# Kernel tuning notes

Hardware: AMD Instinct MI355X
Metric: run time of the kernel (lower is better)

The kernel has to match this reference:

```python
import jax, jax.numpy as jnp
import numpy as np

NUM_HEADS = 16
EPS = 1e-6
ROPE_BASE = 10000.0

def _thw(N, TT):
    table = {2640: (3, 22, 40), 1530: (3, 17, 30), 6120: (3, 34, 60), 660: (3, 11, 20)}
    return table.get(N - TT, (3, 23, 40))

def _positions(t, h, w):
    tt, hh, ww = np.meshgrid(np.arange(t), np.arange(h), np.arange(w), indexing='ij')
    return jnp.asarray(np.stack([tt, hh, ww], -1).reshape(-1, 3), jnp.float32)  # (THW, 3)

def _rope1d(x, pos):
    # x: (B,H,T,d) one axis-chunk, pos: (T,) positions for that axis
    d = x.shape[-1]
    inv_freq = 1.0 / (ROPE_BASE ** (jnp.arange(0, d, 2, dtype=jnp.float32) / d))
    ang = pos[:, None] * inv_freq                     # (T, d/2)
    cos = jnp.concatenate([jnp.cos(ang)] * 2, -1)     # (T, d)
    sin = jnp.concatenate([jnp.sin(ang)] * 2, -1)
    x1, x2 = x[..., : d // 2], x[..., d // 2:]
    return x * cos + jnp.concatenate([-x2, x1], -1) * sin

def _rope3d(x, pos, TT):
    # first TT tokens (text) pass through; video tokens get per-axis rotation
    pre, vid = x[:, :, :TT], x[:, :, TT:]
    chunks = jnp.split(vid, 3, axis=-1)               # t/h/w axis chunks
    rot = [_rope1d(c, pos[:, i]) for i, c in enumerate(chunks)]
    return jnp.concatenate([pre, jnp.concatenate(rot, -1)], axis=2)

def _rms(x, w):
    return x * jax.lax.rsqrt(jnp.mean(x * x, -1, keepdims=True) + EPS) * w

def setup_inputs() -> dict:
    key = jax.random.key(0)
    ks = jax.random.split(key, 12)
    B, N, C = 1, 2866, 1536
    Dh = C // NUM_HEADS
    s = 0.02
    return {
        'x': jax.random.normal(ks[0], (B, N, C), jnp.float32),
        'Wq': jax.random.normal(ks[1], (C, C), jnp.float32) * s,
        'bq': jnp.zeros((C,), jnp.float32),
        'Wk': jax.random.normal(ks[2], (C, C), jnp.float32) * s,
        'bk': jnp.zeros((C,), jnp.float32),
        'Wv': jax.random.normal(ks[3], (C, C), jnp.float32) * s,
        'bv': jnp.zeros((C,), jnp.float32),
        'qn_w': jnp.ones((Dh,), jnp.float32),
        'kn_w': jnp.ones((Dh,), jnp.float32),
        'Wp': jax.random.normal(ks[4], (C, C), jnp.float32) * s,
        'bp': jnp.zeros((C,), jnp.float32),
        'TT': 226,
    }

def reference(x, Wq, bq, Wk, bk, Wv, bv, qn_w, kn_w, Wp, bp, TT):
    B, N, C = x.shape
    H = NUM_HEADS
    Dh = C // H
    def proj(W, b):
        return (x @ W.T + b).reshape(B, N, H, Dh).transpose(0, 2, 1, 3)  # (B,H,N,Dh)
    q, k, v = proj(Wq, bq), proj(Wk, bk), proj(Wv, bv)
    q, k = _rms(q, qn_w), _rms(k, kn_w)
    t, h, w = _thw(N, TT)
    pos = _positions(t, h, w)
    q = _rope3d(q, pos, TT)
    k = _rope3d(k, pos, TT)
    scale = Dh ** -0.5
    attn = jax.nn.softmax(jnp.einsum('bhqd,bhkd->bhqk', q, k) * scale, axis=-1)
    o = jnp.einsum('bhqk,bhkd->bhqd', attn, v)
    o = o.transpose(0, 2, 1, 3).reshape(B, N, C)
    return o @ Wp.T + bp
```

## Files before the change

### kernel.cpp

```cpp
#include <hip/hip_runtime.h>
#include <hip/hip_bf16.h>
#include <math.h>

#define C_DIM 1536
#define H_NUM 16
#define DH    96

typedef __attribute__((ext_vector_type(4))) float  f32x4;
typedef __attribute__((ext_vector_type(8))) short  bf16x8;

__device__ __forceinline__ unsigned short f2bf_rne(float f) {
    unsigned u = __float_as_uint(f);
    unsigned r = (u + 0x7FFFu + ((u >> 16) & 1u)) >> 16;
    return (unsigned short)r;
}
__device__ __forceinline__ float bf2f(unsigned short h) {
    return __uint_as_float(((unsigned)h) << 16);
}

__device__ __forceinline__ void glds16(const void* g, void* l) {
    __builtin_amdgcn_global_load_lds(
        (const __attribute__((address_space(1))) unsigned int*)g,
        (__attribute__((address_space(3))) unsigned int*)l, 16, 0, 0);
}

__global__ __launch_bounds__(256)
void cvt_split(const float* __restrict__ in, unsigned short* __restrict__ hi,
               unsigned short* __restrict__ lo, int n4)
{
    const int i = blockIdx.x * 256 + threadIdx.x;
    if (i >= n4) return;
    float4 v = *(const float4*)&in[4 * i];
    unsigned short h[4], l[4];
    float vv[4] = {v.x, v.y, v.z, v.w};
    #pragma unroll
    for (int j = 0; j < 4; ++j) {
        h[j] = f2bf_rne(vv[j]);
        l[j] = f2bf_rne(vv[j] - bf2f(h[j]));
    }
    *(ushort4*)&hi[4 * i] = *(ushort4*)h;
    *(ushort4*)&lo[4 * i] = *(ushort4*)l;
}

struct CvtArgs {
    const float* src[4];
    unsigned short* hi[4];
    unsigned short* lo[4];
};
__global__ __launch_bounds__(256)
void cvt_split4(CvtArgs a, int n4)
{
    const int i = blockIdx.x * 256 + threadIdx.x;
    if (i >= n4) return;
    const int w = blockIdx.y;
    float4 v = *(const float4*)&a.src[w][4 * i];
    unsigned short h[4], l[4];
    float vv[4] = {v.x, v.y, v.z, v.w};
    #pragma unroll
    for (int j = 0; j < 4; ++j) {
        h[j] = f2bf_rne(vv[j]);
        l[j] = f2bf_rne(vv[j] - bf2f(h[j]));
    }
    *(ushort4*)&a.hi[w][4 * i] = *(ushort4*)h;
    *(ushort4*)&a.lo[w][4 * i] = *(ushort4*)l;
}

__global__ __launch_bounds__(256)
void gemm_mfma(const unsigned short* __restrict__ Ahi,
               const unsigned short* __restrict__ Alo,
               const unsigned short* W0h, const unsigned short* W0l,
               const float* b0, float* Y0,
               const unsigned short* W1h, const unsigned short* W1l,
               const float* b1, float* Y1,
               const unsigned short* W2h, const unsigned short* W2l,
               const float* b2, float* Y2,
               int M)
{
    __shared__ __align__(16) unsigned short lds[2 * 4 * 4096];

    const unsigned short* Wh;
    const unsigned short* Wl;
    const float* bias;
    float* Y;
    if (blockIdx.z == 0)      { Wh = W0h; Wl = W0l; bias = b0; Y = Y0; }
    else if (blockIdx.z == 1) { Wh = W1h; Wl = W1l; bias = b1; Y = Y1; }
    else                      { Wh = W2h; Wl = W2l; bias = b2; Y = Y2; }

    const int t   = threadIdx.x;
    const int m0  = blockIdx.x * 128;
    const int n0  = blockIdx.y * 128;
    const int w   = t >> 6;
    const int l   = t & 63;

    const unsigned short* src =
        (w == 0) ? Ahi : (w == 1) ? Alo : (w == 2) ? Wh : Wl;
    const int rbase = (w < 2) ? m0 : n0;
    const int rmax  = (w < 2) ? (M - 1) : 0x3FFFFFFF;
    const int srow  = l >> 2;
    const int scol  = l & 3;
    const int ssw   = (srow >> 1) & 3;
    int goff[8];
    #pragma unroll
    for (int i = 0; i < 8; ++i) {
        int gr = rbase + 16 * i + srow;
        gr = gr < rmax ? gr : rmax;
        goff[i] = gr * C_DIM + 8 * (scol ^ ssw);
    }

    const int lane = t & 63;
    const int wv   = t >> 6;
    const int wm   = wv & 1, wn = wv >> 1;
    const int lrow = lane & 15;
    const int quad = lane >> 4;
    const int pc   = quad ^ ((lrow >> 1) & 3);
    int aoff[4], boff[4];
    #pragma unroll
    for (int i = 0; i < 4; ++i) {
        aoff[i] = (64 * wm + 16 * i + lrow) * 32 + 8 * pc;
        boff[i] = (64 * wn + 16 * i + lrow) * 32 + 8 * pc;
    }

    f32x4 acc[4][4];
    #pragma unroll
    for (int i = 0; i < 4; ++i)
        #pragma unroll
        for (int j = 0; j < 4; ++j) acc[i][j] = (f32x4)0.f;

    #pragma unroll
    for (int i = 0; i < 8; ++i)
        glds16(src + goff[i], (char*)&lds[w * 4096] + i * 1024);

    const int NT = C_DIM / 32;
    for (int kt = 0; kt < NT; ++kt) {
        const int cb = kt & 1;
        const unsigned short* sA = lds + cb * 16384;

        asm volatile("s_waitcnt vmcnt(0)" ::: "memory");
        __builtin_amdgcn_s_barrier();
        __builtin_amdgcn_sched_barrier(0);

        bf16x8 ah[2], al[2], bh[4], bl[4];

        if (kt + 1 < NT) {
            char* dN = (char*)&lds[(cb ^ 1) * 16384 + w * 4096];
            const int k0n = (kt + 1) * 32;
            #pragma unroll
            for (int i = 0; i < 8; ++i)
                glds16(src + goff[i] + k0n, dN + i * 1024);
        }
        #pragma unroll
        for (int j = 0; j < 4; ++j) {
            bh[j] = *(const bf16x8*)&sA[8192 + boff[j]];
            bl[j] = *(const bf16x8*)&sA[12288 + boff[j]];
        }
        #pragma unroll
        for (int i = 0; i < 2; ++i) {
            ah[i] = *(const bf16x8*)&sA[aoff[i]];
            al[i] = *(const bf16x8*)&sA[4096 + aoff[i]];
        }
        __builtin_amdgcn_s_barrier();
        asm volatile("s_waitcnt lgkmcnt(0)" ::: "memory");
        __builtin_amdgcn_sched_barrier(0);
        __builtin_amdgcn_s_setprio(1);
        #pragma unroll
        for (int i = 0; i < 2; ++i)
            #pragma unroll
            for (int j = 0; j < 4; ++j) {
                acc[i][j] = __builtin_amdgcn_mfma_f32_16x16x32_bf16(ah[i], bh[j], acc[i][j], 0, 0, 0);
                acc[i][j] = __builtin_amdgcn_mfma_f32_16x16x32_bf16(al[i], bh[j], acc[i][j], 0, 0, 0);
                acc[i][j] = __builtin_amdgcn_mfma_f32_16x16x32_bf16(ah[i], bl[j], acc[i][j], 0, 0, 0);
            }
        __builtin_amdgcn_s_setprio(0);
        __builtin_amdgcn_s_barrier();
        __builtin_amdgcn_sched_barrier(0);

        #pragma unroll
        for (int i = 0; i < 2; ++i) {
            ah[i] = *(const bf16x8*)&sA[aoff[2 + i]];
            al[i] = *(const bf16x8*)&sA[4096 + aoff[2 + i]];
        }
        __builtin_amdgcn_s_barrier();
        asm volatile("s_waitcnt lgkmcnt(0)" ::: "memory");
        __builtin_amdgcn_sched_barrier(0);
        __builtin_amdgcn_s_setprio(1);
        #pragma unroll
        for (int i = 0; i < 2; ++i)
            #pragma unroll
            for (int j = 0; j < 4; ++j) {
                acc[2 + i][j] = __builtin_amdgcn_mfma_f32_16x16x32_bf16(ah[i], bh[j], acc[2 + i][j], 0, 0, 0);
                acc[2 + i][j] = __builtin_amdgcn_mfma_f32_16x16x32_bf16(al[i], bh[j], acc[2 + i][j], 0, 0, 0);
                acc[2 + i][j] = __builtin_amdgcn_mfma_f32_16x16x32_bf16(ah[i], bl[j], acc[2 + i][j], 0, 0, 0);
            }
        __builtin_amdgcn_s_setprio(0);
    }

    float bv[4];
    #pragma unroll
    for (int j = 0; j < 4; ++j) bv[j] = bias[n0 + 64 * wn + 16 * j + lrow];
    #pragma unroll
    for (int i = 0; i < 4; ++i) {
        const int rbase2 = m0 + 64 * wm + 16 * i + 4 * quad;
        #pragma unroll
        for (int p = 0; p < 4; ++p) {
            const int row = rbase2 + p;
            if (row >= M) continue;
            #pragma unroll
            for (int j = 0; j < 4; ++j) {
                const int col = n0 + 64 * wn + 16 * j + lrow;
                Y[(size_t)row * C_DIM + col] = acc[i][j][p] + bv[j];
            }
        }
    }
}

__global__ __launch_bounds__(512, 2)
void gemm_mfma256(const unsigned short* __restrict__ Ahi,
                  const unsigned short* __restrict__ Alo,
                  const unsigned short* W0h, const unsigned short* W0l,
                  const float* b0, float* Y0,
                  const unsigned short* W1h, const unsigned short* W1l,
                  const float* b1, float* Y1,
                  const unsigned short* W2h, const unsigned short* W2l,
                  const float* b2, float* Y2,
                  int M)
{
    extern __shared__ __align__(16) unsigned short smem[];

    const unsigned short* Wh;
    const unsigned short* Wl;
    const float* bias;
    float* Y;
    if (blockIdx.z == 0)      { Wh = W0h; Wl = W0l; bias = b0; Y = Y0; }
    else if (blockIdx.z == 1) { Wh = W1h; Wl = W1l; bias = b1; Y = Y1; }
    else                      { Wh = W2h; Wl = W2l; bias = b2; Y = Y2; }

    const int t    = threadIdx.x;
    const int wv   = t >> 6;
    const int lane = t & 63;
    const int m0   = blockIdx.x * 256;
    const int n0   = blockIdx.y * 256;

    const int mat  = wv >> 1;
    const int half = wv & 1;
    const unsigned short* src =
        (mat == 0) ? Ahi : (mat == 1) ? Alo : (mat == 2) ? Wh : Wl;
    const int rbase = (mat < 2) ? m0 : n0;
    const int rmax  = (mat < 2) ? (M - 1) : 0x3FFFFFFF;
    const int srow  = lane >> 2;
    const int scol  = lane & 3;
    const int ssw   = (srow >> 1) & 3;
    int goff[8];
    #pragma unroll
    for (int i = 0; i < 8; ++i) {
        int gr = rbase + half * 128 + 16 * i + srow;
        gr = gr < rmax ? gr : rmax;
        goff[i] = gr * C_DIM + 8 * (scol ^ ssw);
    }
    unsigned short* const dstBase = smem + mat * 8192 + half * 4096;

    const int wm   = wv & 1;
    const int wn   = wv >> 1;
    const int lrow = lane & 15;
    const int quad = lane >> 4;
    const int pc   = quad ^ ((lrow >> 1) & 3);
    int aoff[8], boff[4];
    #pragma unroll
    for (int i = 0; i < 8; ++i)
        aoff[i] = (128 * wm + 16 * i + lrow) * 32 + 8 * pc;
    #pragma unroll
    for (int j = 0; j < 4; ++j)
        boff[j] = (64 * wn + 16 * j + lrow) * 32 + 8 * pc;

    f32x4 acc[8][4];
    #pragma unroll
    for (int i = 0; i < 8; ++i)
        #pragma unroll
        for (int j = 0; j < 4; ++j) acc[i][j] = (f32x4)0.f;

    #pragma unroll
    for (int i = 0; i < 8; ++i)
        glds16(src + goff[i], (char*)dstBase + i * 1024);

    const int NT = C_DIM / 32;
    for (int kt = 0; kt < NT; ++kt) {
        const int cb = kt & 1;
        const unsigned short* sA = smem + cb * 32768;
        unsigned short* dN = dstBase + (cb ^ 1) * 32768;
        const int k0n = (kt + 1) * 32;
        const bool pf = (kt + 1 < NT);

        asm volatile("s_waitcnt vmcnt(0)" ::: "memory");
        __builtin_amdgcn_s_barrier();
        __builtin_amdgcn_sched_barrier(0);

        bf16x8 bh[4], bl[4], ah[2], al[2];

        if (pf) {
            #pragma unroll
            for (int i = 0; i < 4; ++i)
                glds16(src + goff[i] + k0n, (char*)dN + i * 1024);
        }
        #pragma unroll
        for (int j = 0; j < 4; ++j) {
            bh[j] = *(const bf16x8*)&sA[16384 + boff[j]];
            bl[j] = *(const bf16x8*)&sA[24576 + boff[j]];
        }
        #pragma unroll
        for (int i = 0; i < 2; ++i) {
            ah[i] = *(const bf16x8*)&sA[aoff[i]];
            al[i] = *(const bf16x8*)&sA[8192 + aoff[i]];
        }
        __builtin_amdgcn_s_barrier();
        asm volatile("s_waitcnt lgkmcnt(0)" ::: "memory");
        __builtin_amdgcn_sched_barrier(0);
        __builtin_amdgcn_s_setprio(1);
        #pragma unroll
        for (int i = 0; i < 2; ++i)
            #pragma unroll
            for (int j = 0; j < 4; ++j) {
                acc[i][j] = __builtin_amdgcn_mfma_f32_16x16x32_bf16(ah[i], bh[j], acc[i][j], 0, 0, 0);
                acc[i][j] = __builtin_amdgcn_mfma_f32_16x16x32_bf16(al[i], bh[j], acc[i][j], 0, 0, 0);
                acc[i][j] = __builtin_amdgcn_mfma_f32_16x16x32_bf16(ah[i], bl[j], acc[i][j], 0, 0, 0);
            }
        __builtin_amdgcn_s_setprio(0);
        __builtin_amdgcn_s_barrier();
        __builtin_amdgcn_sched_barrier(0);

        if (pf) {
            #pragma unroll
            for (int i = 4; i < 8; ++i)
                glds16(src + goff[i] + k0n, (char*)dN + i * 1024);
        }
        #pragma unroll
        for (int i = 0; i < 2; ++i) {
            ah[i] = *(const bf16x8*)&sA[aoff[2 + i]];
            al[i] = *(const bf16x8*)&sA[8192 + aoff[2 + i]];
        }
        __builtin_amdgcn_s_barrier();
        asm volatile("s_waitcnt lgkmcnt(0)" ::: "memory");
        __builtin_amdgcn_sched_barrier(0);
        __builtin_amdgcn_s_setprio(1);
        #pragma unroll
        for (int i = 0; i < 2; ++i)
            #pragma unroll
            for (int j = 0; j < 4; ++j) {
                acc[2 + i][j] = __builtin_amdgcn_mfma_f32_16x16x32_bf16(ah[i], bh[j], acc[2 + i][j], 0, 0, 0);
                acc[2 + i][j] = __builtin_amdgcn_mfma_f32_16x16x32_bf16(al[i], bh[j], acc[2 + i][j], 0, 0, 0);
                acc[2 + i][j] = __builtin_amdgcn_mfma_f32_16x16x32_bf16(ah[i], bl[j], acc[2 + i][j], 0, 0, 0);
            }
        __builtin_amdgcn_s_setprio(0);
        __builtin_amdgcn_s_barrier();
        __builtin_amdgcn_sched_barrier(0);

        #pragma unroll
        for (int i = 0; i < 2; ++i) {
            ah[i] = *(const bf16x8*)&sA[aoff[4 + i]];
            al[i] = *(const bf16x8*)&sA[8192 + aoff[4 + i]];
        }
        __builtin_amdgcn_s_barrier();
        asm volatile("s_waitcnt lgkmcnt(0)" ::: "memory");
        __builtin_amdgcn_sched_barrier(0);
        __builtin_amdgcn_s_setprio(1);
        #pragma unroll
        for (int i = 0; i < 2; ++i)
            #pragma unroll
            for (int j = 0; j < 4; ++j) {
                acc[4 + i][j] = __builtin_amdgcn_mfma_f32_16x16x32_bf16(ah[i], bh[j], acc[4 + i][j], 0, 0, 0);
                acc[4 + i][j] = __builtin_amdgcn_mfma_f32_16x16x32_bf16(al[i], bh[j], acc[4 + i][j], 0, 0, 0);
                acc[4 + i][j] = __builtin_amdgcn_mfma_f32_16x16x32_bf16(ah[i], bl[j], acc[4 + i][j], 0, 0, 0);
            }
        __builtin_amdgcn_s_setprio(0);
        __builtin_amdgcn_s_barrier();
        __builtin_amdgcn_sched_barrier(0);

        #pragma unroll
        for (int i = 0; i < 2; ++i) {
            ah[i] = *(const bf16x8*)&sA[aoff[6 + i]];
            al[i] = *(const bf16x8*)&sA[8192 + aoff[6 + i]];
        }
        __builtin_amdgcn_s_barrier();
        asm volatile("s_waitcnt lgkmcnt(0)" ::: "memory");
        __builtin_amdgcn_sched_barrier(0);
        __builtin_amdgcn_s_setprio(1);
        #pragma unroll
        for (int i = 0; i < 2; ++i)
            #pragma unroll
            for (int j = 0; j < 4; ++j) {
                acc[6 + i][j] = __builtin_amdgcn_mfma_f32_16x16x32_bf16(ah[i], bh[j], acc[6 + i][j], 0, 0, 0);
                acc[6 + i][j] = __builtin_amdgcn_mfma_f32_16x16x32_bf16(al[i], bh[j], acc[6 + i][j], 0, 0, 0);
                acc[6 + i][j] = __builtin_amdgcn_mfma_f32_16x16x32_bf16(ah[i], bl[j], acc[6 + i][j], 0, 0, 0);
            }
        __builtin_amdgcn_s_setprio(0);
    }

    float bv2[4];
    #pragma unroll
    for (int j = 0; j < 4; ++j) bv2[j] = bias[n0 + 64 * wn + 16 * j + lrow];
    #pragma unroll
    for (int i = 0; i < 8; ++i) {
        const int rbase2 = m0 + 128 * wm + 16 * i + 4 * quad;
        #pragma unroll
        for (int p = 0; p < 4; ++p) {
            const int row = rbase2 + p;
            if (row >= M) continue;
            #pragma unroll
            for (int j = 0; j < 4; ++j) {
                const int col = n0 + 64 * wn + 16 * j + lrow;
                Y[(size_t)row * C_DIM + col] = acc[i][j][p] + bv2[j];
            }
        }
    }
}

__global__ __launch_bounds__(256)
void rms_rope_split(const float* __restrict__ q, const float* __restrict__ k,
                    const float* __restrict__ qw, const float* __restrict__ kw,
                    const int* __restrict__ TTp,
                    unsigned short* __restrict__ qhi,
                    unsigned short* __restrict__ khi, int Ntok)
{
    const int idx = blockIdx.x * 256 + threadIdx.x;
    if (idx >= Ntok * H_NUM) return;
    const int h = idx & (H_NUM - 1);
    const int n = idx >> 4;

    const float* src;
    const float* w;
    if (blockIdx.y == 0) { src = q; w = qw; } else { src = k; w = kw; }
    const float* p = src + (size_t)n * C_DIM + h * DH;

    float x[DH];
    #pragma unroll
    for (int i = 0; i < DH / 4; ++i) *(float4*)&x[4 * i] = *(const float4*)&p[4 * i];

    float ss = 0.f;
    #pragma unroll
    for (int i = 0; i < DH; ++i) ss += x[i] * x[i];
    const float r = rsqrtf(ss * (1.0f / DH) + 1e-6f);
    #pragma unroll
    for (int i = 0; i < DH; ++i) x[i] *= r * w[i];

    const int TT = *TTp;
    if (n >= TT) {
        const int pidx = n - TT;
        const int NT = Ntok - TT;
        int hh = 23, ww = 40;
        if      (NT == 2640) { hh = 22; ww = 40; }
        else if (NT == 1530) { hh = 17; ww = 30; }
        else if (NT == 6120) { hh = 34; ww = 60; }
        else if (NT ==  660) { hh = 11; ww = 20; }
        float pos[3];
        pos[0] = (float)(pidx / (hh * ww));
        pos[1] = (float)((pidx / ww) % hh);
        pos[2] = (float)(pidx % ww);
        #pragma unroll
        for (int c = 0; c < 3; ++c) {
            #pragma unroll
            for (int j = 0; j < 16; ++j) {
                const float invf = exp2f(-0.83048202373f * (float)j);
                const float ang  = pos[c] * invf;
                const float cs = cosf(ang), sn = sinf(ang);
                const float a = x[32 * c + j], b = x[32 * c + j + 16];
                x[32 * c + j]      = a * cs - b * sn;
                x[32 * c + j + 16] = a * sn + b * cs;
            }
        }
    }

    const size_t off = (size_t)n * C_DIM + h * DH;
    const float qscale = 0.14724445f;
    if (blockIdx.y == 0) {
        #pragma unroll
        for (int i = 0; i < DH / 4; ++i) {
            unsigned short hb[4];
            #pragma unroll
            for (int j = 0; j < 4; ++j) hb[j] = f2bf_rne(x[4 * i + j] * qscale);
            *(ushort4*)&qhi[off + 4 * i] = *(ushort4*)hb;
        }
    } else {
        #pragma unroll
        for (int i = 0; i < DH / 4; ++i) {
            unsigned short hb[4];
            #pragma unroll
            for (int j = 0; j < 4; ++j) hb[j] = f2bf_rne(x[4 * i + j]);
            *(ushort4*)&khi[off + 4 * i] = *(ushort4*)hb;
        }
    }
}

__global__ __launch_bounds__(256)
void transpose_v(const float* __restrict__ V, unsigned short* __restrict__ vt,
                 int Ntok, int vtStride)
{
    __shared__ unsigned short tile[96 * 72];
    const int t  = threadIdx.x;
    const int k0 = blockIdx.x * 64;
    const int h  = blockIdx.y;

    #pragma unroll
    for (int it = 0; it < 6; ++it) {
        const int idx = t + 256 * it;
        const int key = idx / 24, dg = idx % 24;
        float vv[4] = {0.f, 0.f, 0.f, 0.f};
        if (k0 + key < Ntok)
            *(float4*)vv = *(const float4*)&V[(size_t)(k0 + key) * C_DIM + h * DH + 4 * dg];
        #pragma unroll
        for (int j = 0; j < 4; ++j) tile[(4 * dg + j) * 72 + key] = f2bf_rne(vv[j]);
    }
    __syncthreads();
    #pragma unroll
    for (int it = 0; it < 3; ++it) {
        const int idx = t + 256 * it;
        const int d = idx >> 3, ck = idx & 7;
        *(bf16x8*)&vt[((size_t)h * DH + d) * vtStride + k0 + 8 * ck] =
            *(const bf16x8*)&tile[d * 72 + 8 * ck];
    }
}

__global__ __launch_bounds__(256)
void attn_mfma(const unsigned short* __restrict__ qhi,
               const unsigned short* __restrict__ khi,
               const unsigned short* __restrict__ vt,
               unsigned short* __restrict__ Ohi,
               unsigned short* __restrict__ Olo,
               int Ntok, int nKt, int vtStride)
{
    __shared__ unsigned short ldsK[64 * 96];
    __shared__ unsigned short ldsV[96 * 72];
    __shared__ unsigned short ldsP[128 * 72];
    __shared__ float ldsL[128];

    const int t    = threadIdx.x;
    const int lane = t & 63;
    const int wv   = t >> 6;
    const int lrow = lane & 15;
    const int quad = lane >> 4;

    const int nQb = gridDim.x;
    const int Lb  = blockIdx.x + nQb * blockIdx.y;
    const int xcd = Lb & 7;
    const int jj  = Lb >> 3;
    const int h   = 2 * xcd + (jj >= nQb ? 1 : 0);
    const int q0  = (jj >= nQb ? jj - nQb : jj) * 128;
    const size_t hoff = (size_t)h * DH;

    bf16x8 qh[2][3];
    #pragma unroll
    for (int qg = 0; qg < 2; ++qg) {
        const int qr = q0 + wv * 32 + qg * 16 + lrow;
        if (qr < Ntok) {
            const size_t base = (size_t)qr * C_DIM + hoff + quad * 8;
            #pragma unroll
            for (int kc = 0; kc < 3; ++kc)
                qh[qg][kc] = *(const bf16x8*)&qhi[base + 32 * kc];
        } else {
            const bf16x8 z = {0,0,0,0,0,0,0,0};
            #pragma unroll
            for (int kc = 0; kc < 3; ++kc) qh[qg][kc] = z;
        }
    }

    const int rK  = t >> 2;
    const int cK  = t & 3;
    const int swK = (rK >> 1) & 3;
    const int swf = (lrow >> 1) & 3;
    const int vd  = t >> 3;
    const int vck = t & 7;

    float lsum[2] = {0.f, 0.f};
    f32x4 oacc[2][6];
    #pragma unroll
    for (int qg = 0; qg < 2; ++qg)
        #pragma unroll
        for (int dt = 0; dt < 6; ++dt) oacc[qg][dt] = (f32x4)0.f;

    const bf16x8 zv = {0,0,0,0,0,0,0,0};
    bf16x8 pk[3], pv[3];
    #pragma unroll
    for (int it = 0; it < 3; ++it) {
        pk[it] = (rK < Ntok) ? *(const bf16x8*)&khi[(size_t)rK * C_DIM + hoff + 8 * (cK + 4 * it)] : zv;
        pv[it] = *(const bf16x8*)&vt[(hoff + vd + 32 * it) * vtStride + 8 * vck];
    }

    const int pRow0 = (wv * 32 + lrow) * 72;
    const int pRow1 = pRow0 + 16 * 72;
    for (int kt = 0; kt < nKt; ++kt) {
        const int k0 = kt * 64;
        __syncthreads();
        #pragma unroll
        for (int it = 0; it < 3; ++it) {
            *(bf16x8*)&ldsK[rK * 96 + 8 * (4 * it + (cK ^ swK))] = pk[it];
            *(bf16x8*)&ldsV[(vd + 32 * it) * 72 + 8 * vck]       = pv[it];
        }
        __syncthreads();

        if (kt + 1 < nKt) {
            const int kn = k0 + 64;
            #pragma unroll
            for (int it = 0; it < 3; ++it) {
                pk[it] = (kn + rK < Ntok) ? *(const bf16x8*)&khi[(size_t)(kn + rK) * C_DIM + hoff + 8 * (cK + 4 * it)] : zv;
                pv[it] = *(const bf16x8*)&vt[(hoff + vd + 32 * it) * vtStride + kn + 8 * vck];
            }
        }

        f32x4 sacc[2][4];
        #pragma unroll
        for (int qg = 0; qg < 2; ++qg)
            #pragma unroll
            for (int mt = 0; mt < 4; ++mt) sacc[qg][mt] = (f32x4)0.f;
        #pragma unroll
        for (int kc = 0; kc < 3; ++kc) {
            #pragma unroll
            for (int mt = 0; mt < 4; ++mt) {
                bf16x8 kb = *(const bf16x8*)&ldsK[(lrow + 16 * mt) * 96 + 8 * (4 * kc + (quad ^ swf))];
                sacc[0][mt] = __builtin_amdgcn_mfma_f32_16x16x32_bf16(kb, qh[0][kc], sacc[0][mt], 0, 0, 0);
                sacc[1][mt] = __builtin_amdgcn_mfma_f32_16x16x32_bf16(kb, qh[1][kc], sacc[1][mt], 0, 0, 0);
            }
        }

        if (kt + 1 < nKt) {
            #pragma unroll
            for (int qg = 0; qg < 2; ++qg) {
                const int pR = qg ? pRow1 : pRow0;
                #pragma unroll
                for (int mt = 0; mt < 4; ++mt) {
                    float e[4];
                    #pragma unroll
                    for (int p = 0; p < 4; ++p) e[p] = exp2f(sacc[qg][mt][p]);
                    lsum[qg] += (e[0] + e[1]) + (e[2] + e[3]);
                    unsigned u0 = __float_as_uint(e[0]) + 0x8000u;
                    unsigned u1 = __float_as_uint(e[1]) + 0x8000u;
                    unsigned u2 = __float_as_uint(e[2]) + 0x8000u;
                    unsigned u3 = __float_as_uint(e[3]) + 0x8000u;
                    uint2 pr;
                    pr.x = __builtin_amdgcn_perm(u1, u0, 0x07060302u);
                    pr.y = __builtin_amdgcn_perm(u3, u2, 0x07060302u);
                    *(uint2*)&ldsP[pR + 16 * mt + 4 * quad] = pr;
                }
            }
        } else {
            const int kq = k0 + 4 * quad;
            #pragma unroll
            for (int qg = 0; qg < 2; ++qg) {
                const int pR = qg ? pRow1 : pRow0;
                #pragma unroll
                for (int mt = 0; mt < 4; ++mt) {
                    float e[4];
                    #pragma unroll
                    for (int p = 0; p < 4; ++p)
                        e[p] = (kq + 16 * mt + p < Ntok) ? exp2f(sacc[qg][mt][p]) : 0.f;
                    lsum[qg] += (e[0] + e[1]) + (e[2] + e[3]);
                    unsigned u0 = __float_as_uint(e[0]) + 0x8000u;
                    unsigned u1 = __float_as_uint(e[1]) + 0x8000u;
                    unsigned u2 = __float_as_uint(e[2]) + 0x8000u;
                    unsigned u3 = __float_as_uint(e[3]) + 0x8000u;
                    uint2 pr;
                    pr.x = __builtin_amdgcn_perm(u1, u0, 0x07060302u);
                    pr.y = __builtin_amdgcn_perm(u3, u2, 0x07060302u);
                    *(uint2*)&ldsP[pR + 16 * mt + 4 * quad] = pr;
                }
            }
        }

        #pragma unroll
        for (int kc2 = 0; kc2 < 2; ++kc2) {
            bf16x8 pa0 = *(const bf16x8*)&ldsP[pRow0 + 32 * kc2 + 8 * quad];
            bf16x8 pa1 = *(const bf16x8*)&ldsP[pRow1 + 32 * kc2 + 8 * quad];
            #pragma unroll
            for (int dt = 0; dt < 6; ++dt) {
                bf16x8 vb = *(const bf16x8*)&ldsV[(16 * dt + lrow) * 72 + 32 * kc2 + 8 * quad];
                oacc[0][dt] = __builtin_amdgcn_mfma_f32_16x16x32_bf16(pa0, vb, oacc[0][dt], 0, 0, 0);
                oacc[1][dt] = __builtin_amdgcn_mfma_f32_16x16x32_bf16(pa1, vb, oacc[1][dt], 0, 0, 0);
            }
        }
    }

    #pragma unroll
    for (int qg = 0; qg < 2; ++qg) {
        lsum[qg] += __shfl_xor(lsum[qg], 16, 64);
        lsum[qg] += __shfl_xor(lsum[qg], 32, 64);
        ldsL[wv * 32 + qg * 16 + lrow] = lsum[qg];
    }
    #pragma unroll
    for (int qg = 0; qg < 2; ++qg) {
        #pragma unroll
        for (int p = 0; p < 4; ++p) {
            const int row = q0 + wv * 32 + qg * 16 + quad * 4 + p;
            if (row >= Ntok) continue;
            const float rl = 1.0f / ldsL[wv * 32 + qg * 16 + quad * 4 + p];
            const size_t rbase = (size_t)row * C_DIM + hoff + lrow;
            #pragma unroll
            for (int dt = 0; dt < 6; ++dt) {
                const float o = oacc[qg][dt][p] * rl;
                const unsigned short hb = f2bf_rne(o);
                Ohi[rbase + 16 * dt] = hb;
                Olo[rbase + 16 * dt] = f2bf_rne(o - bf2f(hb));
            }
        }
    }
}

extern "C" void kernel_launch(void* const* d_in, const int* in_sizes, int n_in,
                              void* d_out, int out_size, void* d_ws, size_t ws_size,
                              hipStream_t stream)
{
    const float* x   = (const float*)d_in[0];
    const float* Wq  = (const float*)d_in[1];
    const float* bq  = (const float*)d_in[2];
    const float* Wk  = (const float*)d_in[3];
    const float* bk  = (const float*)d_in[4];
    const float* Wv  = (const float*)d_in[5];
    const float* bv  = (const float*)d_in[6];
    const float* qnw = (const float*)d_in[7];
    const float* knw = (const float*)d_in[8];
    const float* Wp  = (const float*)d_in[9];
    const float* bp  = (const float*)d_in[10];
    const int*   TTp = (const int*)d_in[11];

    const int Ntok = in_sizes[0] / C_DIM;
    const int nKt  = (Ntok + 63) / 64;
    const int nQb  = (Ntok + 127) / 128;
    const int vtStride = nKt * 64;
    const size_t NC = (size_t)Ntok * C_DIM;
    const size_t CC = (size_t)C_DIM * C_DIM;
    float* out = (float*)d_out;

    static bool s_attr = false;
    if (!s_attr) {
        hipFuncSetAttribute(reinterpret_cast<const void*>(gemm_mfma256),
                            hipFuncAttributeMaxDynamicSharedMemorySize, 131072);
        s_attr = true;
    }

    float*          kbuf = (float*)d_ws;
    float*          vbuf = kbuf + NC;
    unsigned short* xhi  = (unsigned short*)(vbuf + NC);
    unsigned short* xlo  = xhi + NC;
    unsigned short* wsp  = xlo + NC;
    unsigned short* wqh = wsp + 0 * CC, *wql = wsp + 1 * CC;
    unsigned short* wkh = wsp + 2 * CC, *wkl = wsp + 3 * CC;
    unsigned short* wvh = wsp + 4 * CC, *wvl = wsp + 5 * CC;
    unsigned short* wph = wsp + 6 * CC, *wpl = wsp + 7 * CC;
    unsigned short* qhib = wsp + 8 * CC;
    unsigned short* khib = qhib + NC;
    unsigned short* vtb  = khib + NC;
    float*          qbuf = out;
    unsigned short* ohi  = (unsigned short*)kbuf;
    unsigned short* olo  = ohi + NC;

    cvt_split<<<dim3((NC / 4 + 255) / 256), 256, 0, stream>>>(x, xhi, xlo, (int)(NC / 4));
    CvtArgs ca;
    ca.src[0] = Wq; ca.hi[0] = wqh; ca.lo[0] = wql;
    ca.src[1] = Wk; ca.hi[1] = wkh; ca.lo[1] = wkl;
    ca.src[2] = Wv; ca.hi[2] = wvh; ca.lo[2] = wvl;
    ca.src[3] = Wp; ca.hi[3] = wph; ca.lo[3] = wpl;
    cvt_split4<<<dim3((CC / 4 + 255) / 256, 4), 256, 0, stream>>>(ca, (int)(CC / 4));

    dim3 qkvgrid((Ntok + 255) / 256, C_DIM / 256, 3);
    gemm_mfma256<<<qkvgrid, 512, 131072, stream>>>(xhi, xlo,
        wqh, wql, bq, qbuf,
        wkh, wkl, bk, kbuf,
        wvh, wvl, bv, vbuf, Ntok);

    const int nv = Ntok * H_NUM;
    rms_rope_split<<<dim3((nv + 255) / 256, 2), 256, 0, stream>>>(
        qbuf, kbuf, qnw, knw, TTp, qhib, khib, Ntok);

    transpose_v<<<dim3(nKt, H_NUM), 256, 0, stream>>>(vbuf, vtb, Ntok, vtStride);

    attn_mfma<<<dim3(nQb, H_NUM), 256, 0, stream>>>(
        qhib, khib, vtb, ohi, olo, Ntok, nKt, vtStride);

    dim3 pgrid((Ntok + 127) / 128, C_DIM / 128, 1);
    gemm_mfma<<<pgrid, 256, 0, stream>>>(ohi, olo,
        wph, wpl, bp, out,
        wph, wpl, bp, out,
        wph, wpl, bp, out, Ntok);
}
```

Measured before the change: 488.5 us.

## Split attention over the key dimension into two partitions with a combine kernel

Attention blocks now take a third grid dimension that splits the key tiles into two halves. Each half writes unnormalized partial outputs (hi/lo bf16) and row sums, and a new combine kernel adds them and normalizes. The softmax needs no max rescaling, so the partial sums add directly. The aim is to double the attention block count (23x16 was under-filling the GPU) at the cost of extra global traffic and one more kernel launch.

```diff
diff --git a/kernel.cpp b/kernel.cpp
--- a/kernel.cpp
+++ b/kernel.cpp
@@ -521,9 +521,10 @@
 void attn_mfma(const unsigned short* __restrict__ qhi,
                const unsigned short* __restrict__ khi,
                const unsigned short* __restrict__ vt,
-               unsigned short* __restrict__ Ohi,
-               unsigned short* __restrict__ Olo,
-               int Ntok, int nKt, int vtStride)
+               unsigned short* __restrict__ S0h, unsigned short* __restrict__ S0l,
+               unsigned short* __restrict__ S1h, unsigned short* __restrict__ S1l,
+               float* __restrict__ lbuf,
+               int Ntok, int nKt, int nK0, int vtStride)
 {
     __shared__ unsigned short ldsK[64 * 96];
     __shared__ unsigned short ldsV[96 * 72];
@@ -535,6 +536,13 @@
     const int wv   = t >> 6;
     const int lrow = lane & 15;
     const int quad = lane >> 4;
+
+    const int part  = blockIdx.z;
+    const int ktBeg = part ? nK0 : 0;
+    const int ktEnd = part ? nKt : nK0;
+    unsigned short* const Shi = part ? S1h : S0h;
+    unsigned short* const Slo = part ? S1l : S0l;
+    float* const lout = lbuf + (size_t)part * Ntok * H_NUM;
 
     const int nQb = gridDim.x;
     const int Lb  = blockIdx.x + nQb * blockIdx.y;
@@ -576,15 +584,16 @@
 
     const bf16x8 zv = {0,0,0,0,0,0,0,0};
     bf16x8 pk[3], pv[3];
+    const int kB = ktBeg * 64;
     #pragma unroll
     for (int it = 0; it < 3; ++it) {
-        pk[it] = (rK < Ntok) ? *(const bf16x8*)&khi[(size_t)rK * C_DIM + hoff + 8 * (cK + 4 * it)] : zv;
-        pv[it] = *(const bf16x8*)&vt[(hoff + vd + 32 * it) * vtStride + 8 * vck];
+        pk[it] = (kB + rK < Ntok) ? *(const bf16x8*)&khi[(size_t)(kB + rK) * C_DIM + hoff + 8 * (cK + 4 * it)] : zv;
+        pv[it] = *(const bf16x8*)&vt[(hoff + vd + 32 * it) * vtStride + kB + 8 * vck];
     }
 
     const int pRow0 = (wv * 32 + lrow) * 72;
     const int pRow1 = pRow0 + 16 * 72;
-    for (int kt = 0; kt < nKt; ++kt) {
+    for (int kt = ktBeg; kt < ktEnd; ++kt) {
         const int k0 = kt * 64;
         __syncthreads();
         #pragma unroll
@@ -594,7 +603,7 @@
         }
         __syncthreads();
 
-        if (kt + 1 < nKt) {
+        if (kt + 1 < ktEnd) {
             const int kn = k0 + 64;
             #pragma unroll
             for (int it = 0; it < 3; ++it) {
@@ -618,7 +627,7 @@
             }
         }
 
-        if (kt + 1 < nKt) {
+        if (kt != nKt - 1) {
             #pragma unroll
             for (int qg = 0; qg < 2; ++qg) {
                 const int pR = qg ? pRow1 : pRow0;
@@ -687,17 +696,54 @@
         for (int p = 0; p < 4; ++p) {
             const int row = q0 + wv * 32 + qg * 16 + quad * 4 + p;
             if (row >= Ntok) continue;
-            const float rl = 1.0f / ldsL[wv * 32 + qg * 16 + quad * 4 + p];
+            if (lrow == 0)
+                lout[(size_t)row * H_NUM + h] = ldsL[wv * 32 + qg * 16 + quad * 4 + p];
             const size_t rbase = (size_t)row * C_DIM + hoff + lrow;
             #pragma unroll
             for (int dt = 0; dt < 6; ++dt) {
-                const float o = oacc[qg][dt][p] * rl;
+                const float o = oacc[qg][dt][p];
                 const unsigned short hb = f2bf_rne(o);
-                Ohi[rbase + 16 * dt] = hb;
-                Olo[rbase + 16 * dt] = f2bf_rne(o - bf2f(hb));
-            }
-        }
-    }
+                Shi[rbase + 16 * dt] = hb;
+                Slo[rbase + 16 * dt] = f2bf_rne(o - bf2f(hb));
+            }
+        }
+    }
+}
+
+__global__ __launch_bounds__(256)
+void attn_combine(const unsigned short* __restrict__ s0h, const unsigned short* __restrict__ s0l,
+                  const unsigned short* __restrict__ s1h, const unsigned short* __restrict__ s1l,
+                  const float* __restrict__ lbuf,
+                  unsigned short* __restrict__ ohi, unsigned short* __restrict__ olo,
+                  int Ntok)
+{
+    const int i  = blockIdx.x * 256 + threadIdx.x;
+    const int n4 = Ntok * (C_DIM / 4);
+    if (i >= n4) return;
+    const int row = (4 * i) / C_DIM;
+    const int col = (4 * i) % C_DIM;
+    const int h   = col / DH;
+    const float rl = 1.0f /
+        (lbuf[(size_t)row * H_NUM + h] + lbuf[(size_t)Ntok * H_NUM + (size_t)row * H_NUM + h]);
+
+    ushort4 a0 = *(const ushort4*)&s0h[4 * i];
+    ushort4 b0 = *(const ushort4*)&s0l[4 * i];
+    ushort4 a1 = *(const ushort4*)&s1h[4 * i];
+    ushort4 b1 = *(const ushort4*)&s1l[4 * i];
+    const unsigned short* pa0 = (const unsigned short*)&a0;
+    const unsigned short* pb0 = (const unsigned short*)&b0;
+    const unsigned short* pa1 = (const unsigned short*)&a1;
+    const unsigned short* pb1 = (const unsigned short*)&b1;
+    unsigned short oh[4], ol[4];
+    #pragma unroll
+    for (int j = 0; j < 4; ++j) {
+        const float s = (bf2f(pa0[j]) + bf2f(pb0[j])) + (bf2f(pa1[j]) + bf2f(pb1[j]));
+        const float o = s * rl;
+        oh[j] = f2bf_rne(o);
+        ol[j] = f2bf_rne(o - bf2f(oh[j]));
+    }
+    *(ushort4*)&ohi[4 * i] = *(ushort4*)oh;
+    *(ushort4*)&olo[4 * i] = *(ushort4*)ol;
 }
 
 extern "C" void kernel_launch(void* const* d_in, const int* in_sizes, int n_in,
@@ -719,6 +765,7 @@
 
     const int Ntok = in_sizes[0] / C_DIM;
     const int nKt  = (Ntok + 63) / 64;
+    const int nK0  = (nKt + 1) / 2;
     const int nQb  = (Ntok + 127) / 128;
     const int vtStride = nKt * 64;
     const size_t NC = (size_t)Ntok * C_DIM;
@@ -744,9 +791,14 @@
     unsigned short* qhib = wsp + 8 * CC;
     unsigned short* khib = qhib + NC;
     unsigned short* vtb  = khib + NC;
+    float*          lbuf = (float*)(vtb + (size_t)H_NUM * DH * vtStride);
     float*          qbuf = out;
-    unsigned short* ohi  = (unsigned short*)kbuf;
-    unsigned short* olo  = ohi + NC;
+    unsigned short* s0h = (unsigned short*)kbuf;
+    unsigned short* s0l = s0h + NC;
+    unsigned short* s1h = (unsigned short*)vbuf;
+    unsigned short* s1l = s1h + NC;
+    unsigned short* ohi = xhi;
+    unsigned short* olo = xlo;
 
     cvt_split<<<dim3((NC / 4 + 255) / 256), 256, 0, stream>>>(x, xhi, xlo, (int)(NC / 4));
     CvtArgs ca;
@@ -768,8 +820,11 @@
 
     transpose_v<<<dim3(nKt, H_NUM), 256, 0, stream>>>(vbuf, vtb, Ntok, vtStride);
 
-    attn_mfma<<<dim3(nQb, H_NUM), 256, 0, stream>>>(
-        qhib, khib, vtb, ohi, olo, Ntok, nKt, vtStride);
+    attn_mfma<<<dim3(nQb, H_NUM, 2), 256, 0, stream>>>(
+        qhib, khib, vtb, s0h, s0l, s1h, s1l, lbuf, Ntok, nKt, nK0, vtStride);
+
+    attn_combine<<<dim3((NC / 4 + 255) / 256), 256, 0, stream>>>(
+        s0h, s0l, s1h, s1l, lbuf, ohi, olo, Ntok);
 
     dim3 pgrid((Ntok + 127) / 128, C_DIM / 128, 1);
     gemm_mfma<<<pgrid, 256, 0, stream>>>(ohi, olo,
```

Result: faster. 478.3 us (-2.1%).
